# Kernel tuning notes

Measured on AMD Instinct MI355X. Metric: run time of the kernel, lower is better.

The kernel has to match this reference:

```python
import jax, jax.numpy as jnp
import numpy as np

B, T, C = 4, 128, 512
NH, HS = 8, 64          # n_head, head_dim = C // NH
ORDER = 3               # attention_order
SCALE = 1.0 / np.sqrt(HS)


def setup_inputs() -> dict:
    key = jax.random.key(0)
    ks = jax.random.split(key, 7)
    s = 0.02
    return {
        "x": jax.random.normal(ks[0], (B, T, C), jnp.float32),
        "Wp0": jax.random.normal(ks[1], (C, C), jnp.float32) * s,
        "Wp1": jax.random.normal(ks[2], (C, C), jnp.float32) * s,
        "Wp2": jax.random.normal(ks[3], (C, C), jnp.float32) * s,
        "Wv0": jax.random.normal(ks[4], (HS, HS), jnp.float32) * s,
        "Wv1": jax.random.normal(ks[5], (HS, HS), jnp.float32) * s,
        "Wc": jax.random.normal(ks[6], (C, C), jnp.float32) * s,
    }


def _heads(x, W):
    # Linear then split heads: (B,T,C) -> (B,NH,T,HS)
    return (x @ W).reshape(B, T, NH, HS).transpose(0, 2, 1, 3)


def _causal_mask(t, order):
    # indices grid [T]^order, True where i0 >= i1 >= ... >= i_{order-1}
    idx = jnp.arange(t)
    g = jnp.stack(jnp.meshgrid(*([idx] * order), indexing='ij'), axis=-1)
    return jnp.all(jnp.diff(g, axis=-1) <= 0, axis=-1)


def reference(x, Wp0, Wp1, Wp2, Wv0, Wv1, Wc):
    p0 = _heads(x, Wp0)  # (B,NH,T,HS)
    p1 = _heads(x, Wp1)
    p2 = _heads(x, Wp2)

    # pairwise scores, then higher-order broadcast exactly as the torch einsum
    # ('bh...i,bhkd->bh...ik' sums the key over d and broadcasts — faithful).
    att = jnp.einsum('bhid,bhjd->bhij', p0, p1) * SCALE        # (B,NH,T,T)
    att = jnp.einsum('bh...i,bhkd->bh...ik', att, p2)          # (B,NH,T,T,T)

    mask = _causal_mask(T, ORDER)[None, None]                  # (1,1,T,T,T)
    att = jnp.where(mask, att, -jnp.inf)
    att = jax.nn.softmax(att.reshape(B, NH, T, T * T), axis=-1)

    # value tensors with broadcasted elementwise product over the order dims
    V0 = (p1 @ Wv0)[:, :, :, None, :]   # (B,NH,T,1,HS)
    V1 = (p2 @ Wv1)[:, :, None, :, :]   # (B,NH,1,T,HS)
    V = (V0 * V1).reshape(B, NH, T * T, HS)

    y = jnp.einsum('bhij,bhjd->bhid', att, V)                  # (B,NH,T,HS)
    y = y.transpose(0, 2, 1, 3).reshape(B, T, C)
    return y @ Wc
```

## Files before the change

### kernel.cpp

```cpp
#include <hip/hip_runtime.h>
#include <hip/hip_bf16.h>
#include <math.h>

#define B 4
#define T 128
#define C 512
#define NH 8
#define HS 64
#define BH (B*NH)

typedef __attribute__((ext_vector_type(8))) short bf16x8;
typedef __attribute__((ext_vector_type(4))) float f32x4;

__device__ __forceinline__ unsigned short bfc(float x) {
    return __builtin_bit_cast(unsigned short, __float2bfloat16(x));
}
__device__ __forceinline__ unsigned int pk_bf16(float a, float b) {
    return (unsigned int)bfc(a) | ((unsigned int)bfc(b) << 16);
}
__device__ __forceinline__ float lo_f(unsigned int g) {
    return __builtin_bit_cast(float, g << 16);
}
__device__ __forceinline__ float hi_f(unsigned int g) {
    return __builtin_bit_cast(float, g & 0xffff0000u);
}

__global__ __launch_bounds__(256) void proj_kernel(
    const float* __restrict__ X,
    const float* __restrict__ Wp0, const float* __restrict__ Wp1, const float* __restrict__ Wp2,
    unsigned short* __restrict__ p0b, unsigned short* __restrict__ p1b,
    unsigned short* __restrict__ p2b, float* __restrict__ rr)
{
    __shared__ __align__(16) unsigned short As[64][72];
    __shared__ __align__(16) unsigned short Bs[64][72];
    __shared__ float Ls[64][69];
    __shared__ float sRS[4][64];
    const int z = blockIdx.z;
    const float* W = (z == 0) ? Wp0 : (z == 1) ? Wp1 : Wp2;
    const int m0 = blockIdx.y * 64, n0 = blockIdx.x * 64;
    const int tid = threadIdx.x;
    const int w = tid >> 6, lane = tid & 63, quad = lane >> 4, l16 = lane & 15;
    f32x4 acc[4];
    #pragma unroll
    for (int mt = 0; mt < 4; ++mt) acc[mt] = (f32x4){0.f, 0.f, 0.f, 0.f};

    for (int k0 = 0; k0 < 512; k0 += 64) {
        __syncthreads();
        #pragma unroll
        for (int it = 0; it < 2; ++it) {
            const int q = tid + it * 256;
            const int row = q >> 3, c8 = (q & 7) * 8;
            const float4 a = *(const float4*)&X[(size_t)(m0 + row) * 512 + k0 + c8];
            const float4 b = *(const float4*)&X[(size_t)(m0 + row) * 512 + k0 + c8 + 4];
            uint4 o;
            o.x = pk_bf16(a.x, a.y);
            o.y = pk_bf16(a.z, a.w);
            o.z = pk_bf16(b.x, b.y);
            o.w = pk_bf16(b.z, b.w);
            *(uint4*)&As[row][c8] = o;
        }
        #pragma unroll
        for (int it = 0; it < 4; ++it) {
            const int q = tid + it * 256;
            const int row = q >> 4, c4 = (q & 15) * 4;
            const float4 v = *(const float4*)&W[(size_t)(k0 + row) * 512 + n0 + c4];
            Ls[row][c4 + 0] = v.x; Ls[row][c4 + 1] = v.y;
            Ls[row][c4 + 2] = v.z; Ls[row][c4 + 3] = v.w;
        }
        __syncthreads();
        #pragma unroll
        for (int it = 0; it < 2; ++it) {
            const int q = tid + it * 256;
            const int nrow = q >> 3, k8 = (q & 7) * 8;
            uint4 o;
            o.x = pk_bf16(Ls[k8 + 0][nrow], Ls[k8 + 1][nrow]);
            o.y = pk_bf16(Ls[k8 + 2][nrow], Ls[k8 + 3][nrow]);
            o.z = pk_bf16(Ls[k8 + 4][nrow], Ls[k8 + 5][nrow]);
            o.w = pk_bf16(Ls[k8 + 6][nrow], Ls[k8 + 7][nrow]);
            *(uint4*)&Bs[nrow][k8] = o;
        }
        __syncthreads();
        #pragma unroll
        for (int kt = 0; kt < 2; ++kt) {
            const bf16x8 b8 = *(const bf16x8*)&Bs[w * 16 + l16][kt * 32 + quad * 8];
            #pragma unroll
            for (int mt = 0; mt < 4; ++mt) {
                const bf16x8 a8 = *(const bf16x8*)&As[mt * 16 + l16][kt * 32 + quad * 8];
                acc[mt] = __builtin_amdgcn_mfma_f32_16x16x32_bf16(a8, b8, acc[mt], 0, 0, 0);
            }
        }
    }

    {
        const int n = n0 + w * 16 + l16;
        const int h = n >> 6, d = n & 63;
        unsigned short* pz = (z == 0) ? p0b : (z == 1) ? p1b : p2b;
        #pragma unroll
        for (int mt = 0; mt < 4; ++mt) {
            #pragma unroll
            for (int r = 0; r < 4; ++r) {
                const int m = m0 + mt * 16 + quad * 4 + r;
                const int bb = m >> 7, t = m & 127;
                pz[((size_t)(bb * NH + h) * T + t) * HS + d] = bfc(acc[mt][r]);
            }
        }
    }
    if (z == 2) {
        #pragma unroll
        for (int mt = 0; mt < 4; ++mt)
            #pragma unroll
            for (int r = 0; r < 4; ++r) {
                float v = acc[mt][r];
                v += __shfl_xor(v, 1, 64); v += __shfl_xor(v, 2, 64);
                v += __shfl_xor(v, 4, 64); v += __shfl_xor(v, 8, 64);
                if (l16 == 0) sRS[w][mt * 16 + quad * 4 + r] = v;
            }
        __syncthreads();
        if (tid < 64) {
            const float s = sRS[0][tid] + sRS[1][tid] + sRS[2][tid] + sRS[3][tid];
            const int m = m0 + tid, bb = m >> 7, tl = m & 127, h = n0 >> 6;
            rr[(bb * NH + h) * T + tl] = s;
        }
    }
}

__global__ __launch_bounds__(256) void attn_kernel(
    const unsigned short* __restrict__ p0b, const unsigned short* __restrict__ p1b,
    const unsigned short* __restrict__ p2b, const float* __restrict__ rr,
    const float* __restrict__ Wv0, const float* __restrict__ Wv1,
    unsigned short* __restrict__ Yb)
{
    __shared__ __align__(16) union {
        struct {
            unsigned short sWv[64][72];
            unsigned short sVst[64][136];
        } v;
        unsigned short sE[2][128 * 128];
    } u;
    __shared__ float sS[8][128];
    __shared__ float srr[128];
    __shared__ float sZ[2][4];

    const int bid = blockIdx.x;
    const int bh = bid & (BH - 1);
    const int ig = bid >> 5;
    const int tid = threadIdx.x;
    const int w = tid >> 6;
    const int lane = tid & 63;
    const int quad = lane >> 4;
    const int l16 = lane & 15;

    if (tid < 128) srr[tid] = rr[bh * T + tid];

    #pragma unroll
    for (int it = 0; it < 4; ++it) {
        const int k = (tid >> 4) + it * 16;
        const int d0 = (tid & 15) * 4;
        const float4 wv = *(const float4*)&Wv0[(size_t)k * 64 + d0];
        u.v.sWv[d0 + 0][k] = bfc(wv.x); u.v.sWv[d0 + 1][k] = bfc(wv.y);
        u.v.sWv[d0 + 2][k] = bfc(wv.z); u.v.sWv[d0 + 3][k] = bfc(wv.w);
    }
    __syncthreads();

    #pragma unroll
    for (int nn = 0; nn < 2; ++nn) {
        const int nt = w + nn * 4;
        f32x4 vacc[4];
        #pragma unroll
        for (int mt = 0; mt < 4; ++mt) vacc[mt] = (f32x4){0.f, 0.f, 0.f, 0.f};
        #pragma unroll
        for (int kt = 0; kt < 2; ++kt) {
            const bf16x8 b8 = *(const bf16x8*)&p1b[((size_t)bh * T + nt * 16 + l16) * HS + kt * 32 + quad * 8];
            #pragma unroll
            for (int mt = 0; mt < 4; ++mt) {
                const bf16x8 a8 = *(const bf16x8*)&u.v.sWv[mt * 16 + l16][kt * 32 + quad * 8];
                vacc[mt] = __builtin_amdgcn_mfma_f32_16x16x32_bf16(a8, b8, vacc[mt], 0, 0, 0);
            }
        }
        #pragma unroll
        for (int mt = 0; mt < 4; ++mt)
            #pragma unroll
            for (int r = 0; r < 4; ++r)
                u.v.sVst[mt * 16 + quad * 4 + r][nt * 16 + l16] = bfc(vacc[mt][r]);
    }
    __syncthreads();

    uint2 v0r[8];
    #pragma unroll
    for (int mt = 0; mt < 8; ++mt)
        v0r[mt] = *(const uint2*)&u.v.sVst[(w << 4) + l16][(mt << 4) + (quad << 2)];
    #pragma unroll
    for (int it = 0; it < 4; ++it) {
        const int k = (tid >> 4) + it * 16;
        const int d0 = (tid & 15) * 4;
        const float4 wv = *(const float4*)&Wv1[(size_t)k * 64 + d0];
        u.v.sWv[d0 + 0][k] = bfc(wv.x); u.v.sWv[d0 + 1][k] = bfc(wv.y);
        u.v.sWv[d0 + 2][k] = bfc(wv.z); u.v.sWv[d0 + 3][k] = bfc(wv.w);
    }
    __syncthreads();

    #pragma unroll
    for (int nn = 0; nn < 2; ++nn) {
        const int nt = w + nn * 4;
        f32x4 vacc[4];
        #pragma unroll
        for (int mt = 0; mt < 4; ++mt) vacc[mt] = (f32x4){0.f, 0.f, 0.f, 0.f};
        #pragma unroll
        for (int kt = 0; kt < 2; ++kt) {
            const bf16x8 b8 = *(const bf16x8*)&p2b[((size_t)bh * T + nt * 16 + l16) * HS + kt * 32 + quad * 8];
            #pragma unroll
            for (int mt = 0; mt < 4; ++mt) {
                const bf16x8 a8 = *(const bf16x8*)&u.v.sWv[mt * 16 + l16][kt * 32 + quad * 8];
                vacc[mt] = __builtin_amdgcn_mfma_f32_16x16x32_bf16(a8, b8, vacc[mt], 0, 0, 0);
            }
        }
        #pragma unroll
        for (int mt = 0; mt < 4; ++mt)
            #pragma unroll
            for (int r = 0; r < 4; ++r)
                u.v.sVst[mt * 16 + quad * 4 + r][nt * 16 + l16] = bfc(vacc[mt][r]);
    }
    __syncthreads();

    uint4 v1r[4];
    #pragma unroll
    for (int kt = 0; kt < 4; ++kt)
        v1r[kt] = *(const uint4*)&u.v.sVst[(w << 4) + l16][(quad << 3) + (kt << 5)];
    {
        const int qr = l16 & 7;
        const int irow = (qr & 1) ? (16 * qr + 15 - ig) : (16 * qr + ig);
        const unsigned short* ap = p0b + ((size_t)bh * T + irow) * HS + (quad << 3);
        const unsigned short* bp = p1b + (size_t)bh * T * HS + (quad << 3);
        f32x4 s0 = (f32x4){0.f, 0.f, 0.f, 0.f};
        f32x4 s1 = (f32x4){0.f, 0.f, 0.f, 0.f};
        #pragma unroll
        for (int kt = 0; kt < 2; ++kt) {
            const bf16x8 a8 = *(const bf16x8*)(ap + (kt << 5));
            const bf16x8 b0 = *(const bf16x8*)(bp + (size_t)((w << 5) + l16) * HS + (kt << 5));
            const bf16x8 b1 = *(const bf16x8*)(bp + (size_t)((w << 5) + 16 + l16) * HS + (kt << 5));
            s0 = __builtin_amdgcn_mfma_f32_16x16x32_bf16(a8, b0, s0, 0, 0, 0);
            s1 = __builtin_amdgcn_mfma_f32_16x16x32_bf16(a8, b1, s1, 0, 0, 0);
        }
        if (quad < 2) {
            #pragma unroll
            for (int r = 0; r < 4; ++r) {
                sS[quad * 4 + r][(w << 5) + l16]      = s0[r] * 0.125f;
                sS[quad * 4 + r][(w << 5) + 16 + l16] = s1[r] * 0.125f;
            }
        }
    }
    __syncthreads();

    const float L2E = 1.4426950408889634f;

    float mhat;
    {
        float aS = 0.f;
        #pragma unroll
        for (int q = 0; q < 8; ++q) {
            aS = fmaxf(aS, fabsf(sS[q][lane]));
            aS = fmaxf(aS, fabsf(sS[q][64 + lane]));
        }
        float aR = fmaxf(fabsf(srr[lane]), fabsf(srr[64 + lane]));
        #pragma unroll
        for (int off = 32; off; off >>= 1) {
            aS = fmaxf(aS, __shfl_xor(aS, off, 64));
            aR = fmaxf(aR, __shfl_xor(aR, off, 64));
        }
        mhat = aS * aR;
    }
    const float bexp = -mhat * L2E;
    const int cc = tid & 15;
    const int rowin = tid >> 4;
    const int k0l = cc << 3;
    float rk[8];
    *(float4*)&rk[0] = *(const float4*)&srr[k0l];
    *(float4*)&rk[4] = *(const float4*)&srr[k0l + 4];

    for (int qq = 7; qq >= 0; --qq) {
        const int i = (qq & 1) ? (16 * qq + 15 - ig) : (16 * qq + ig);
        const float* sSq = sS[qq];
        const int mtmax = i >> 4;
        const int buf = qq & 1;
        float zacc = 0.f;

        const int npass = mtmax + 1;
        for (int p = 0; p < npass; ++p) {
            const int jj = (p << 4) + rowin;
            uint4 o = {0u, 0u, 0u, 0u};
            if (jj <= i && k0l <= jj) {
                const float aL = sSq[jj] * L2E;
                const int dlim = jj - k0l;
                float e[8];
                #pragma unroll
                for (int q = 0; q < 8; ++q) {
                    const float ex = __builtin_amdgcn_exp2f(fmaf(aL, rk[q], bexp));
                    e[q] = (q <= dlim) ? ex : 0.f;
                    zacc += e[q];
                }
                o.x = pk_bf16(e[0], e[1]);
                o.y = pk_bf16(e[2], e[3]);
                o.z = pk_bf16(e[4], e[5]);
                o.w = pk_bf16(e[6], e[7]);
            }
            *(uint4*)&u.sE[buf][(jj << 7) + ((cc ^ (jj & 7)) << 3)] = o;
        }
        #pragma unroll
        for (int off = 32; off; off >>= 1) zacc += __shfl_xor(zacc, off, 64);
        if (lane == 0) sZ[buf][w] = zacc;
        __syncthreads();

        f32x4 acc[8];
        #pragma unroll
        for (int mt = 0; mt < 8; ++mt) acc[mt] = (f32x4){0.f, 0.f, 0.f, 0.f};
        #pragma unroll
        for (int mt = 0; mt < 8; ++mt) {
            if (mt <= mtmax) {
                #pragma unroll
                for (int kt = 0; kt < 4; ++kt) {
                    if (kt <= (mt >> 1)) {
                        const int ch = ((kt << 2) + quad) ^ (l16 & 7);
                        const bf16x8 a8 = *(const bf16x8*)&u.sE[buf][(((mt << 4) + l16) << 7) + (ch << 3)];
                        acc[mt] = __builtin_amdgcn_mfma_f32_16x16x32_bf16(
                            a8, __builtin_bit_cast(bf16x8, v1r[kt]), acc[mt], 0, 0, 0);
                    }
                }
            }
        }
        const float Z = sZ[buf][0] + sZ[buf][1] + sZ[buf][2] + sZ[buf][3];

        float part = 0.f;
        #pragma unroll
        for (int mt = 0; mt < 8; ++mt) {
            if (mt < mtmax) {
                const uint2 uu = v0r[mt];
                part = fmaf(lo_f(uu.x), acc[mt][0], part);
                part = fmaf(hi_f(uu.x), acc[mt][1], part);
                part = fmaf(lo_f(uu.y), acc[mt][2], part);
                part = fmaf(hi_f(uu.y), acc[mt][3], part);
            } else if (mt == mtmax) {
                const uint2 uu = v0r[mt];
                const int jb = (mt << 4) + (quad << 2);
                if (jb + 0 <= i) part = fmaf(lo_f(uu.x), acc[mt][0], part);
                if (jb + 1 <= i) part = fmaf(hi_f(uu.x), acc[mt][1], part);
                if (jb + 2 <= i) part = fmaf(lo_f(uu.y), acc[mt][2], part);
                if (jb + 3 <= i) part = fmaf(hi_f(uu.y), acc[mt][3], part);
            }
        }
        part += __shfl_xor(part, 16, 64);
        part += __shfl_xor(part, 32, 64);
        if (lane < 16) {
            const int bb = bh >> 3, hh = bh & 7;
            Yb[((size_t)(bb * T + i) * C) + hh * HS + (w << 4) + l16] = bfc(part / Z);
        }
    }
}

__global__ __launch_bounds__(256) void outmm_kernel(
    const unsigned short* __restrict__ Ab, const float* __restrict__ Wc,
    float* __restrict__ OUT)
{
    __shared__ __align__(16) unsigned short As[64][72];
    __shared__ __align__(16) unsigned short Bs[64][72];
    __shared__ float Ls[64][69];
    const int m0 = blockIdx.y * 64, n0 = blockIdx.x * 64;
    const int tid = threadIdx.x;
    const int w = tid >> 6, lane = tid & 63, quad = lane >> 4, l16 = lane & 15;
    f32x4 acc[4];
    #pragma unroll
    for (int mt = 0; mt < 4; ++mt) acc[mt] = (f32x4){0.f, 0.f, 0.f, 0.f};
    for (int k0 = 0; k0 < 512; k0 += 64) {
        __syncthreads();
        #pragma unroll
        for (int it = 0; it < 2; ++it) {
            const int q = tid + it * 256;
            const int row = q >> 3, c8 = (q & 7) * 8;
            *(uint4*)&As[row][c8] = *(const uint4*)&Ab[(size_t)(m0 + row) * 512 + k0 + c8];
        }
        #pragma unroll
        for (int it = 0; it < 4; ++it) {
            const int q = tid + it * 256;
            const int row = q >> 4, c4 = (q & 15) * 4;
            const float4 v = *(const float4*)&Wc[(size_t)(k0 + row) * 512 + n0 + c4];
            Ls[row][c4 + 0] = v.x; Ls[row][c4 + 1] = v.y;
            Ls[row][c4 + 2] = v.z; Ls[row][c4 + 3] = v.w;
        }
        __syncthreads();
        #pragma unroll
        for (int it = 0; it < 2; ++it) {
            const int q = tid + it * 256;
            const int nrow = q >> 3, k8 = (q & 7) * 8;
            uint4 o;
            o.x = pk_bf16(Ls[k8 + 0][nrow], Ls[k8 + 1][nrow]);
            o.y = pk_bf16(Ls[k8 + 2][nrow], Ls[k8 + 3][nrow]);
            o.z = pk_bf16(Ls[k8 + 4][nrow], Ls[k8 + 5][nrow]);
            o.w = pk_bf16(Ls[k8 + 6][nrow], Ls[k8 + 7][nrow]);
            *(uint4*)&Bs[nrow][k8] = o;
        }
        __syncthreads();
        #pragma unroll
        for (int kt = 0; kt < 2; ++kt) {
            const bf16x8 b8 = *(const bf16x8*)&Bs[w * 16 + l16][kt * 32 + quad * 8];
            #pragma unroll
            for (int mt = 0; mt < 4; ++mt) {
                const bf16x8 a8 = *(const bf16x8*)&As[mt * 16 + l16][kt * 32 + quad * 8];
                acc[mt] = __builtin_amdgcn_mfma_f32_16x16x32_bf16(a8, b8, acc[mt], 0, 0, 0);
            }
        }
    }
    const int n = n0 + w * 16 + l16;
    #pragma unroll
    for (int mt = 0; mt < 4; ++mt)
        #pragma unroll
        for (int r = 0; r < 4; ++r) {
            const int mrow = m0 + mt * 16 + quad * 4 + r;
            OUT[(size_t)mrow * 512 + n] = acc[mt][r];
        }
}

extern "C" void kernel_launch(void* const* d_in, const int* in_sizes, int n_in,
                              void* d_out, int out_size, void* d_ws, size_t ws_size,
                              hipStream_t stream)
{
    const float* x   = (const float*)d_in[0];
    const float* Wp0 = (const float*)d_in[1];
    const float* Wp1 = (const float*)d_in[2];
    const float* Wp2 = (const float*)d_in[3];
    const float* Wv0 = (const float*)d_in[4];
    const float* Wv1 = (const float*)d_in[5];
    const float* Wc  = (const float*)d_in[6];
    float* out = (float*)d_out;

    char* w8 = (char*)d_ws;
    const size_t HB = 512 * 1024;
    unsigned short* p0b = (unsigned short*)(w8 + 0 * HB);
    unsigned short* p1b = (unsigned short*)(w8 + 1 * HB);
    unsigned short* p2b = (unsigned short*)(w8 + 2 * HB);
    unsigned short* Yb  = (unsigned short*)(w8 + 3 * HB);
    float*          rr  = (float*)        (w8 + 4 * HB);

    proj_kernel <<<dim3(8, 8, 3), 256, 0, stream>>>(x, Wp0, Wp1, Wp2, p0b, p1b, p2b, rr);
    attn_kernel <<<dim3(512), 256, 0, stream>>>(p0b, p1b, p2b, rr, Wv0, Wv1, Yb);
    outmm_kernel<<<dim3(8, 8), 256, 0, stream>>>(Yb, Wc, out);
}
```

Before: 118.0 us.

## Double attention block to 512 threads and split the PV tiles across wave halves

Raises the attention kernel from 4 to 8 waves per block. Each wave computes one 16-column tile of the value projections and scores, and the E-tile build now takes half as many passes. The two wave halves each take four of the eight M-tiles in the P·V MMA, and their partial outputs are reduced through shared memory in a final epilogue. The aim is more latency hiding and parallel work per block, at the cost of extra shared memory for partial sums, more register pressure under launch_bounds(512,4), and a final reduction step.

```diff
diff --git a/kernel.cpp b/kernel.cpp
--- a/kernel.cpp
+++ b/kernel.cpp
@@ -124,7 +124,7 @@
     }
 }
 
-__global__ __launch_bounds__(256) void attn_kernel(
+__global__ __launch_bounds__(512, 4) void attn_kernel(
     const unsigned short* __restrict__ p0b, const unsigned short* __restrict__ p1b,
     const unsigned short* __restrict__ p2b, const float* __restrict__ rr,
     const float* __restrict__ Wv0, const float* __restrict__ Wv1,
@@ -139,7 +139,8 @@
     } u;
     __shared__ float sS[8][128];
     __shared__ float srr[128];
-    __shared__ float sZ[2][4];
+    __shared__ float sZarr[8][8];
+    __shared__ float sY[8][2][64];
 
     const int bid = blockIdx.x;
     const int bh = bid & (BH - 1);
@@ -149,12 +150,14 @@
     const int lane = tid & 63;
     const int quad = lane >> 4;
     const int l16 = lane & 15;
+    const int wq = w & 3;
+    const int h4 = (w >> 2) * 4;
 
     if (tid < 128) srr[tid] = rr[bh * T + tid];
 
     #pragma unroll
-    for (int it = 0; it < 4; ++it) {
-        const int k = (tid >> 4) + it * 16;
+    for (int it = 0; it < 2; ++it) {
+        const int k = (tid >> 4) + it * 32;
         const int d0 = (tid & 15) * 4;
         const float4 wv = *(const float4*)&Wv0[(size_t)k * 64 + d0];
         u.v.sWv[d0 + 0][k] = bfc(wv.x); u.v.sWv[d0 + 1][k] = bfc(wv.y);
@@ -162,15 +165,13 @@
     }
     __syncthreads();
 
-    #pragma unroll
-    for (int nn = 0; nn < 2; ++nn) {
-        const int nt = w + nn * 4;
+    {
         f32x4 vacc[4];
         #pragma unroll
         for (int mt = 0; mt < 4; ++mt) vacc[mt] = (f32x4){0.f, 0.f, 0.f, 0.f};
         #pragma unroll
         for (int kt = 0; kt < 2; ++kt) {
-            const bf16x8 b8 = *(const bf16x8*)&p1b[((size_t)bh * T + nt * 16 + l16) * HS + kt * 32 + quad * 8];
+            const bf16x8 b8 = *(const bf16x8*)&p1b[((size_t)bh * T + w * 16 + l16) * HS + kt * 32 + quad * 8];
             #pragma unroll
             for (int mt = 0; mt < 4; ++mt) {
                 const bf16x8 a8 = *(const bf16x8*)&u.v.sWv[mt * 16 + l16][kt * 32 + quad * 8];
@@ -181,17 +182,17 @@
         for (int mt = 0; mt < 4; ++mt)
             #pragma unroll
             for (int r = 0; r < 4; ++r)
-                u.v.sVst[mt * 16 + quad * 4 + r][nt * 16 + l16] = bfc(vacc[mt][r]);
-    }
-    __syncthreads();
-
-    uint2 v0r[8];
-    #pragma unroll
-    for (int mt = 0; mt < 8; ++mt)
-        v0r[mt] = *(const uint2*)&u.v.sVst[(w << 4) + l16][(mt << 4) + (quad << 2)];
-    #pragma unroll
-    for (int it = 0; it < 4; ++it) {
-        const int k = (tid >> 4) + it * 16;
+                u.v.sVst[mt * 16 + quad * 4 + r][w * 16 + l16] = bfc(vacc[mt][r]);
+    }
+    __syncthreads();
+
+    uint2 v0r[4];
+    #pragma unroll
+    for (int m = 0; m < 4; ++m)
+        v0r[m] = *(const uint2*)&u.v.sVst[(wq << 4) + l16][((h4 + m) << 4) + (quad << 2)];
+    #pragma unroll
+    for (int it = 0; it < 2; ++it) {
+        const int k = (tid >> 4) + it * 32;
         const int d0 = (tid & 15) * 4;
         const float4 wv = *(const float4*)&Wv1[(size_t)k * 64 + d0];
         u.v.sWv[d0 + 0][k] = bfc(wv.x); u.v.sWv[d0 + 1][k] = bfc(wv.y);
@@ -199,15 +200,13 @@
     }
     __syncthreads();
 
-    #pragma unroll
-    for (int nn = 0; nn < 2; ++nn) {
-        const int nt = w + nn * 4;
+    {
         f32x4 vacc[4];
         #pragma unroll
         for (int mt = 0; mt < 4; ++mt) vacc[mt] = (f32x4){0.f, 0.f, 0.f, 0.f};
         #pragma unroll
         for (int kt = 0; kt < 2; ++kt) {
-            const bf16x8 b8 = *(const bf16x8*)&p2b[((size_t)bh * T + nt * 16 + l16) * HS + kt * 32 + quad * 8];
+            const bf16x8 b8 = *(const bf16x8*)&p2b[((size_t)bh * T + w * 16 + l16) * HS + kt * 32 + quad * 8];
             #pragma unroll
             for (int mt = 0; mt < 4; ++mt) {
                 const bf16x8 a8 = *(const bf16x8*)&u.v.sWv[mt * 16 + l16][kt * 32 + quad * 8];
@@ -218,35 +217,30 @@
         for (int mt = 0; mt < 4; ++mt)
             #pragma unroll
             for (int r = 0; r < 4; ++r)
-                u.v.sVst[mt * 16 + quad * 4 + r][nt * 16 + l16] = bfc(vacc[mt][r]);
+                u.v.sVst[mt * 16 + quad * 4 + r][w * 16 + l16] = bfc(vacc[mt][r]);
     }
     __syncthreads();
 
     uint4 v1r[4];
     #pragma unroll
     for (int kt = 0; kt < 4; ++kt)
-        v1r[kt] = *(const uint4*)&u.v.sVst[(w << 4) + l16][(quad << 3) + (kt << 5)];
+        v1r[kt] = *(const uint4*)&u.v.sVst[(wq << 4) + l16][(quad << 3) + (kt << 5)];
     {
         const int qr = l16 & 7;
         const int irow = (qr & 1) ? (16 * qr + 15 - ig) : (16 * qr + ig);
         const unsigned short* ap = p0b + ((size_t)bh * T + irow) * HS + (quad << 3);
         const unsigned short* bp = p1b + (size_t)bh * T * HS + (quad << 3);
         f32x4 s0 = (f32x4){0.f, 0.f, 0.f, 0.f};
-        f32x4 s1 = (f32x4){0.f, 0.f, 0.f, 0.f};
         #pragma unroll
         for (int kt = 0; kt < 2; ++kt) {
             const bf16x8 a8 = *(const bf16x8*)(ap + (kt << 5));
-            const bf16x8 b0 = *(const bf16x8*)(bp + (size_t)((w << 5) + l16) * HS + (kt << 5));
-            const bf16x8 b1 = *(const bf16x8*)(bp + (size_t)((w << 5) + 16 + l16) * HS + (kt << 5));
+            const bf16x8 b0 = *(const bf16x8*)(bp + (size_t)((w << 4) + l16) * HS + (kt << 5));
             s0 = __builtin_amdgcn_mfma_f32_16x16x32_bf16(a8, b0, s0, 0, 0, 0);
-            s1 = __builtin_amdgcn_mfma_f32_16x16x32_bf16(a8, b1, s1, 0, 0, 0);
         }
         if (quad < 2) {
             #pragma unroll
-            for (int r = 0; r < 4; ++r) {
-                sS[quad * 4 + r][(w << 5) + l16]      = s0[r] * 0.125f;
-                sS[quad * 4 + r][(w << 5) + 16 + l16] = s1[r] * 0.125f;
-            }
+            for (int r = 0; r < 4; ++r)
+                sS[quad * 4 + r][(w << 4) + l16] = s0[r] * 0.125f;
         }
     }
     __syncthreads();
@@ -284,9 +278,9 @@
         const int buf = qq & 1;
         float zacc = 0.f;
 
-        const int npass = mtmax + 1;
+        const int npass = (mtmax + 2) >> 1;
         for (int p = 0; p < npass; ++p) {
-            const int jj = (p << 4) + rowin;
+            const int jj = (p << 5) + rowin;
             uint4 o = {0u, 0u, 0u, 0u};
             if (jj <= i && k0l <= jj) {
                 const float aL = sSq[jj] * L2E;
@@ -307,52 +301,63 @@
         }
         #pragma unroll
         for (int off = 32; off; off >>= 1) zacc += __shfl_xor(zacc, off, 64);
-        if (lane == 0) sZ[buf][w] = zacc;
-        __syncthreads();
-
-        f32x4 acc[8];
-        #pragma unroll
-        for (int mt = 0; mt < 8; ++mt) acc[mt] = (f32x4){0.f, 0.f, 0.f, 0.f};
-        #pragma unroll
-        for (int mt = 0; mt < 8; ++mt) {
+        if (lane == 0) sZarr[qq][w] = zacc;
+        __syncthreads();
+
+        f32x4 acc[4];
+        #pragma unroll
+        for (int m = 0; m < 4; ++m) acc[m] = (f32x4){0.f, 0.f, 0.f, 0.f};
+        #pragma unroll
+        for (int mtl = 0; mtl < 4; ++mtl) {
+            const int mt = h4 + mtl;
             if (mt <= mtmax) {
                 #pragma unroll
                 for (int kt = 0; kt < 4; ++kt) {
                     if (kt <= (mt >> 1)) {
                         const int ch = ((kt << 2) + quad) ^ (l16 & 7);
                         const bf16x8 a8 = *(const bf16x8*)&u.sE[buf][(((mt << 4) + l16) << 7) + (ch << 3)];
-                        acc[mt] = __builtin_amdgcn_mfma_f32_16x16x32_bf16(
-                            a8, __builtin_bit_cast(bf16x8, v1r[kt]), acc[mt], 0, 0, 0);
+                        acc[mtl] = __builtin_amdgcn_mfma_f32_16x16x32_bf16(
+                            a8, __builtin_bit_cast(bf16x8, v1r[kt]), acc[mtl], 0, 0, 0);
                     }
                 }
             }
         }
-        const float Z = sZ[buf][0] + sZ[buf][1] + sZ[buf][2] + sZ[buf][3];
 
         float part = 0.f;
         #pragma unroll
-        for (int mt = 0; mt < 8; ++mt) {
+        for (int mtl = 0; mtl < 4; ++mtl) {
+            const int mt = h4 + mtl;
             if (mt < mtmax) {
-                const uint2 uu = v0r[mt];
-                part = fmaf(lo_f(uu.x), acc[mt][0], part);
-                part = fmaf(hi_f(uu.x), acc[mt][1], part);
-                part = fmaf(lo_f(uu.y), acc[mt][2], part);
-                part = fmaf(hi_f(uu.y), acc[mt][3], part);
+                const uint2 uu = v0r[mtl];
+                part = fmaf(lo_f(uu.x), acc[mtl][0], part);
+                part = fmaf(hi_f(uu.x), acc[mtl][1], part);
+                part = fmaf(lo_f(uu.y), acc[mtl][2], part);
+                part = fmaf(hi_f(uu.y), acc[mtl][3], part);
             } else if (mt == mtmax) {
-                const uint2 uu = v0r[mt];
+                const uint2 uu = v0r[mtl];
                 const int jb = (mt << 4) + (quad << 2);
-                if (jb + 0 <= i) part = fmaf(lo_f(uu.x), acc[mt][0], part);
-                if (jb + 1 <= i) part = fmaf(hi_f(uu.x), acc[mt][1], part);
-                if (jb + 2 <= i) part = fmaf(lo_f(uu.y), acc[mt][2], part);
-                if (jb + 3 <= i) part = fmaf(hi_f(uu.y), acc[mt][3], part);
+                if (jb + 0 <= i) part = fmaf(lo_f(uu.x), acc[mtl][0], part);
+                if (jb + 1 <= i) part = fmaf(hi_f(uu.x), acc[mtl][1], part);
+                if (jb + 2 <= i) part = fmaf(lo_f(uu.y), acc[mtl][2], part);
+                if (jb + 3 <= i) part = fmaf(hi_f(uu.y), acc[mtl][3], part);
             }
         }
         part += __shfl_xor(part, 16, 64);
         part += __shfl_xor(part, 32, 64);
-        if (lane < 16) {
-            const int bb = bh >> 3, hh = bh & 7;
-            Yb[((size_t)(bb * T + i) * C) + hh * HS + (w << 4) + l16] = bfc(part / Z);
-        }
+        if (lane < 16) sY[qq][w >> 2][(wq << 4) + l16] = part;
+    }
+
+    __syncthreads();
+    {
+        const int qq = w;
+        const int d = lane;
+        const int i = (qq & 1) ? (16 * qq + 15 - ig) : (16 * qq + ig);
+        float Z = 0.f;
+        #pragma unroll
+        for (int ww = 0; ww < 8; ++ww) Z += sZarr[qq][ww];
+        const float y = sY[qq][0][d] + sY[qq][1][d];
+        const int bb = bh >> 3, hh = bh & 7;
+        Yb[((size_t)(bb * T + i) * C) + hh * HS + d] = bfc(y / Z);
     }
 }
 
@@ -440,6 +445,6 @@
     float*          rr  = (float*)        (w8 + 4 * HB);
 
     proj_kernel <<<dim3(8, 8, 3), 256, 0, stream>>>(x, Wp0, Wp1, Wp2, p0b, p1b, p2b, rr);
-    attn_kernel <<<dim3(512), 256, 0, stream>>>(p0b, p1b, p2b, rr, Wv0, Wv1, Yb);
+    attn_kernel <<<dim3(512), 512, 0, stream>>>(p0b, p1b, p2b, rr, Wv0, Wv1, Yb);
     outmm_kernel<<<dim3(8, 8), 256, 0, stream>>>(Yb, Wc, out);
 }
```

Measured after the change: 113.8 us. -3.5%, faster.
